# Kernel tuning notes

Measured on AMD Instinct MI355X. Metric: run time of the kernel, lower is better.

The kernel has to match this reference:

```python
import jax, jax.numpy as jnp
import numpy as np
from jax import lax

DIL_R = 2            # dilation_radius
K = 2 * DIL_R + 1    # 5x5 morphology kernel
FOCAL_ALPHA = 0.25
FOCAL_GAMMA = 2.0
BOUNDARY_W = 1.0
IGNORE_IDX = 250


def setup_inputs() -> dict:
    key = jax.random.key(0)
    k1, k2 = jax.random.split(key)
    pred = jax.random.normal(k1, (32, 2, 512, 512), dtype=jnp.float32)
    target = jax.random.randint(k2, (32, 512, 512), 0, 2, dtype=jnp.int64)
    return {"pred": pred, "target": target}


def _boundary_mask(target):
    # labels float, 5x5 all-ones conv with 'same' padding (zero pad),
    # dilated = (conv > 0), eroded = (-conv(-x) > K*K-1) == (conv(x) > K*K-1)
    x = target.astype(jnp.float32)[:, None]                    # [B,1,H,W]
    kern = jnp.ones((1, 1, K, K), dtype=jnp.float32)
    s = lax.conv_general_dilated(x, kern, (1, 1), 'SAME',
                                 dimension_numbers=('NCHW', 'OIHW', 'NCHW'))
    dilated = (s > 0).astype(jnp.float32)
    eroded = (s > (K * K - 1)).astype(jnp.float32)
    return (dilated - eroded)[:, 0]                            # [B,H,W]


def _loss(pred, target, boundary):
    logp = jax.nn.log_softmax(pred, axis=1)                    # [B,2,H,W]
    # per-pixel CE
    ce_pix = -jnp.take_along_axis(logp, target[:, None].astype(jnp.int32), axis=1)[:, 0]  # [B,H,W]
    # main CE with ignore_index=250
    valid = (target != IGNORE_IDX)
    ce_loss = jnp.sum(ce_pix * valid) / jnp.maximum(jnp.sum(valid), 1)
    # focal loss (no ignore, mean over all pixels)
    pt = jnp.exp(-ce_pix)
    focal = jnp.mean(FOCAL_ALPHA * (1.0 - pt) ** FOCAL_GAMMA * ce_pix)
    # boundary dice on class-1 prob
    prob1 = jnp.exp(logp[:, 1])                                # softmax(pred,1)[:,1]
    tgt_f = target.astype(jnp.float32)
    bp = prob1 * boundary
    bt = tgt_f * boundary
    inter = jnp.sum(bp * bt, axis=(1, 2))
    union = jnp.sum(bp, axis=(1, 2)) + jnp.sum(bt, axis=(1, 2))
    dice = 2.0 * inter / (union + 1e-8)
    bdice = 1.0 - jnp.mean(dice)
    return ce_loss + BOUNDARY_W * focal + BOUNDARY_W * bdice


def reference(pred, target):
    boundary = _boundary_mask(target)
    return _loss(pred, target, boundary)
```

## Files before the change

### kernel.cpp

```cpp
#include <hip/hip_runtime.h>
#include <math.h>

#define BATCH 32
#define HH 512
#define WW 512
#define TW 64
#define TH 16
#define HALO 2
#define SW (TW + 2*HALO)
#define SH (TH + 2*HALO)
#define NTILEX (WW / TW)
#define NTILEY (HH / TH)
#define NPIX ((float)BATCH * HH * WW)

#define SLOT(j,b) ((((j) * BATCH) + (b)) * 32)
#define WS_FLOATS (6 * BATCH * 32)

__global__ void zero_ws_kernel(float* ws) {
    int i = blockIdx.x * 256 + threadIdx.x;
    if (i < WS_FLOATS) ws[i] = 0.0f;
}

__global__ __launch_bounds__(256) void bel_main_kernel(
        const float* __restrict__ pred,
        const int*   __restrict__ target,
        float*       __restrict__ ws) {
    __shared__ int   stgt[SH][SW];
    __shared__ int   hsum[SH][TW];
    __shared__ float red[6][4];

    const int tid = threadIdx.x;
    const int bid = blockIdx.x;
    const int bx = bid % NTILEX;
    const int by = (bid / NTILEX) % NTILEY;
    const int b  = bid / (NTILEX * NTILEY);

    const int gx0 = bx * TW - HALO;
    const int gy0 = by * TH - HALO;
    const int tb  = b * HH * WW;

    for (int i = tid; i < SH * SW; i += 256) {
        int r = i / SW, c = i - r * SW;
        int gy = gy0 + r, gx = gx0 + c;
        int v = 0;
        if ((unsigned)gy < (unsigned)HH && (unsigned)gx < (unsigned)WW)
            v = target[tb + gy * WW + gx];
        stgt[r][c] = v;
    }
    __syncthreads();

    for (int i = tid; i < SH * TW; i += 256) {
        int r = i >> 6, c = i & 63;
        hsum[r][c] = stgt[r][c] + stgt[r][c+1] + stgt[r][c+2]
                   + stgt[r][c+3] + stgt[r][c+4];
    }
    __syncthreads();

    const int tx = tid & 63;
    const int ty = tid >> 6;

    float ce_acc = 0.f, cnt_acc = 0.f, focal_acc = 0.f;
    float inter_acc = 0.f, bp_acc = 0.f, bt_acc = 0.f;

    #pragma unroll
    for (int k = 0; k < TH / 4; ++k) {
        const int yl = ty + 4 * k;
        const int y  = by * TH + yl;
        const int x  = bx * TW + tx;

        const int s = hsum[yl][tx] + hsum[yl+1][tx] + hsum[yl+2][tx]
                    + hsum[yl+3][tx] + hsum[yl+4][tx];
        const float bm = (s > 0 && s <= 24) ? 1.0f : 0.0f;

        const int t = stgt[yl + HALO][tx + HALO];

        const int pix = y * WW + x;
        const float p0 = pred[2*tb + pix];
        const float p1 = pred[2*tb + HH*WW + pix];

        const float m   = fmaxf(p0, p1);
        const float d   = fabsf(p0 - p1);
        const float lse = m + __logf(1.0f + __expf(-d));

        const int   tc = (t < 0) ? 0 : ((t > 1) ? 1 : t);
        const float pt_logit = tc ? p1 : p0;
        const float ce = lse - pt_logit;

        const float valid = (t != 250) ? 1.0f : 0.0f;
        ce_acc  += ce * valid;
        cnt_acc += valid;

        const float pt  = __expf(-ce);
        const float omp = 1.0f - pt;
        focal_acc += 0.25f * omp * omp * ce;

        const float prob1 = __expf(p1 - lse);
        const float bp = prob1 * bm;
        const float bt = (float)t * bm;
        inter_acc += bp * bt;
        bp_acc    += bp;
        bt_acc    += bt;
    }

    float vals[6] = {ce_acc, cnt_acc, focal_acc, inter_acc, bp_acc, bt_acc};
    #pragma unroll
    for (int j = 0; j < 6; ++j) {
        float v = vals[j];
        #pragma unroll
        for (int off = 32; off > 0; off >>= 1)
            v += __shfl_down(v, off, 64);
        vals[j] = v;
    }
    const int wave = tid >> 6;
    const int lane = tid & 63;
    if (lane == 0) {
        #pragma unroll
        for (int j = 0; j < 6; ++j) red[j][wave] = vals[j];
    }
    __syncthreads();
    if (tid == 0) {
        #pragma unroll
        for (int j = 0; j < 6; ++j) {
            vals[j] = red[j][0] + red[j][1] + red[j][2] + red[j][3];
            atomicAdd(&ws[SLOT(j, b)], vals[j]);
        }
    }
}

__global__ void bel_finalize_kernel(const float* __restrict__ ws,
                                    float* __restrict__ out) {
    const int t = threadIdx.x;
    float ce_p = 0.f, cnt_p = 0.f, focal_p = 0.f, dice_p = 0.f;
    if (t < BATCH) {
        ce_p    = ws[SLOT(0, t)];
        cnt_p   = ws[SLOT(1, t)];
        focal_p = ws[SLOT(2, t)];
        const float inter = ws[SLOT(3, t)];
        const float uni   = ws[SLOT(4, t)] + ws[SLOT(5, t)];
        dice_p = 2.0f * inter / (uni + 1e-8f);
    }
    #pragma unroll
    for (int off = 32; off > 0; off >>= 1) {
        ce_p    += __shfl_down(ce_p, off, 64);
        cnt_p   += __shfl_down(cnt_p, off, 64);
        focal_p += __shfl_down(focal_p, off, 64);
        dice_p  += __shfl_down(dice_p, off, 64);
    }
    if (t == 0) {
        const float ce_loss = ce_p / fmaxf(cnt_p, 1.0f);
        const float focal   = focal_p / NPIX;
        const float bdice   = 1.0f - dice_p / (float)BATCH;
        out[0] = ce_loss + focal + bdice;
    }
}

extern "C" void kernel_launch(void* const* d_in, const int* in_sizes, int n_in,
                              void* d_out, int out_size, void* d_ws, size_t ws_size,
                              hipStream_t stream) {
    const float* pred   = (const float*)d_in[0];
    const int*   target = (const int*)d_in[1];
    float* ws  = (float*)d_ws;
    float* out = (float*)d_out;

    zero_ws_kernel<<<(WS_FLOATS + 255) / 256, 256, 0, stream>>>(ws);
    bel_main_kernel<<<NTILEX * NTILEY * BATCH, 256, 0, stream>>>(pred, target, ws);
    bel_finalize_kernel<<<1, 64, 0, stream>>>(ws, out);
}
```

Baseline: 134.5 us.

## Use full-row tiles with byte-packed labels and SWAR box sums

Measured after the change: 118.7 us. 1.13x faster.

```diff
diff --git a/kernel.cpp b/kernel.cpp
--- a/kernel.cpp
+++ b/kernel.cpp
@@ -4,14 +4,13 @@
 #define BATCH 32
 #define HH 512
 #define WW 512
-#define TW 64
 #define TH 16
 #define HALO 2
-#define SW (TW + 2*HALO)
-#define SH (TH + 2*HALO)
-#define NTILEX (WW / TW)
-#define NTILEY (HH / TH)
+#define SRH (TH + 2*HALO)
+#define NDW (WW / 4)
+#define CSTRIDE 132
 #define NPIX ((float)BATCH * HH * WW)
+#define HW (HH * WW)
 
 #define SLOT(j,b) ((((j) * BATCH) + (b)) * 32)
 #define WS_FLOATS (6 * BATCH * 32)
@@ -25,104 +24,133 @@
         const float* __restrict__ pred,
         const int*   __restrict__ target,
         float*       __restrict__ ws) {
-    __shared__ int   stgt[SH][SW];
-    __shared__ int   hsum[SH][TW];
+    __shared__ unsigned int t8[SRH][NDW];
+    __shared__ unsigned int csum[TH][CSTRIDE];
     __shared__ float red[6][4];
 
     const int tid = threadIdx.x;
     const int bid = blockIdx.x;
-    const int bx = bid % NTILEX;
-    const int by = (bid / NTILEX) % NTILEY;
-    const int b  = bid / (NTILEX * NTILEY);
+    const int b   = bid >> 5;
+    const int ty  = bid & 31;
+    const int y0  = ty * TH;
+    const size_t tb = (size_t)b * HW;
 
-    const int gx0 = bx * TW - HALO;
-    const int gy0 = by * TH - HALO;
-    const int tb  = b * HH * WW;
+    if (tid < 2 * TH) {
+        int rr = tid >> 1;
+        csum[rr][(tid & 1) ? (NDW + 1) : 0] = 0u;
+    }
 
-    for (int i = tid; i < SH * SW; i += 256) {
-        int r = i / SW, c = i - r * SW;
-        int gy = gy0 + r, gx = gx0 + c;
-        int v = 0;
-        if ((unsigned)gy < (unsigned)HH && (unsigned)gx < (unsigned)WW)
-            v = target[tb + gy * WW + gx];
-        stgt[r][c] = v;
+    #pragma unroll
+    for (int it = 0; it < (SRH * NDW) / 256; ++it) {
+        const int i  = tid + 256 * it;
+        const int r  = i >> 7;
+        const int c4 = i & 127;
+        const int gy = y0 - HALO + r;
+        unsigned int packed = 0u;
+        if ((unsigned)gy < (unsigned)HH) {
+            const int4 v = *(const int4*)(target + tb + ((size_t)gy << 9) + (c4 << 2));
+            packed = (unsigned)v.x | ((unsigned)v.y << 8)
+                   | ((unsigned)v.z << 16) | ((unsigned)v.w << 24);
+        }
+        t8[r][c4] = packed;
     }
     __syncthreads();
 
-    for (int i = tid; i < SH * TW; i += 256) {
-        int r = i >> 6, c = i & 63;
-        hsum[r][c] = stgt[r][c] + stgt[r][c+1] + stgt[r][c+2]
-                   + stgt[r][c+3] + stgt[r][c+4];
+    #pragma unroll
+    for (int it = 0; it < (TH * NDW) / 256; ++it) {
+        const int j = tid + 256 * it;
+        const int r = j >> 7;
+        const int c = j & 127;
+        csum[r][c + 1] = t8[r][c] + t8[r+1][c] + t8[r+2][c]
+                       + t8[r+3][c] + t8[r+4][c];
     }
     __syncthreads();
 
-    const int tx = tid & 63;
-    const int ty = tid >> 6;
+    const float4* __restrict__ pr0 = (const float4*)(pred + tb * 2);
+    const float4* __restrict__ pr1 = (const float4*)(pred + tb * 2 + HW);
 
     float ce_acc = 0.f, cnt_acc = 0.f, focal_acc = 0.f;
     float inter_acc = 0.f, bp_acc = 0.f, bt_acc = 0.f;
 
-    #pragma unroll
-    for (int k = 0; k < TH / 4; ++k) {
-        const int yl = ty + 4 * k;
-        const int y  = by * TH + yl;
-        const int x  = bx * TW + tx;
+    const unsigned long long M5 = 0xFFFFFFFFFFull;
+    const unsigned long long ALL5 = 0x0505050505ull;
 
-        const int s = hsum[yl][tx] + hsum[yl+1][tx] + hsum[yl+2][tx]
-                    + hsum[yl+3][tx] + hsum[yl+4][tx];
-        const float bm = (s > 0 && s <= 24) ? 1.0f : 0.0f;
+    for (int it = 0; it < (TH * NDW) / 256; ++it) {
+        const int j = tid + 256 * it;
+        const int r = j >> 7;
+        const int g = j & 127;
+        const int y = y0 + r;
+        const int fidx = (y << 7) + g;
 
-        const int t = stgt[yl + HALO][tx + HALO];
+        const float4 f0 = pr0[fidx];
+        const float4 f1 = pr1[fidx];
 
-        const int pix = y * WW + x;
-        const float p0 = pred[2*tb + pix];
-        const float p1 = pred[2*tb + HH*WW + pix];
+        const unsigned int L = csum[r][g];
+        const unsigned int M = csum[r][g + 1];
+        const unsigned int R = csum[r][g + 2];
+        const unsigned int tdw = t8[r + HALO][g];
 
-        const float m   = fmaxf(p0, p1);
-        const float d   = fabsf(p0 - p1);
-        const float lse = m + __logf(1.0f + __expf(-d));
+        const unsigned long long lo  = (unsigned long long)L | ((unsigned long long)M << 32);
+        const unsigned long long mid = (unsigned long long)M | ((unsigned long long)R << 32);
 
-        const int   tc = (t < 0) ? 0 : ((t > 1) ? 1 : t);
-        const float pt_logit = tc ? p1 : p0;
-        const float ce = lse - pt_logit;
+        #pragma unroll
+        for (int i = 0; i < 4; ++i) {
+            unsigned long long w;
+            if      (i == 0) w = (lo  >> 16) & M5;
+            else if (i == 1) w = (lo  >> 24) & M5;
+            else if (i == 2) w =  mid        & M5;
+            else             w = (mid >>  8) & M5;
+            const float bm = (w != 0ull && w != ALL5) ? 1.0f : 0.0f;
 
-        const float valid = (t != 250) ? 1.0f : 0.0f;
-        ce_acc  += ce * valid;
-        cnt_acc += valid;
+            const unsigned int tv = (tdw >> (8 * i)) & 0xFFu;
 
-        const float pt  = __expf(-ce);
-        const float omp = 1.0f - pt;
-        focal_acc += 0.25f * omp * omp * ce;
+            const float p0 = (i == 0) ? f0.x : (i == 1) ? f0.y : (i == 2) ? f0.z : f0.w;
+            const float p1 = (i == 0) ? f1.x : (i == 1) ? f1.y : (i == 2) ? f1.z : f1.w;
 
-        const float prob1 = __expf(p1 - lse);
-        const float bp = prob1 * bm;
-        const float bt = (float)t * bm;
-        inter_acc += bp * bt;
-        bp_acc    += bp;
-        bt_acc    += bt;
+            const float d  = p1 - p0;
+            const float e  = __expf(-fabsf(d));
+            const float rz = 1.0f / (1.0f + e);
+            const float pmin = e * rz;
+            const float prob1 = (d >= 0.0f) ? rz : pmin;
+            const float pt = tv ? prob1 : (1.0f - prob1);
+            const float ce = -__logf(pt);
+
+            const float valid = (tv != 250u) ? 1.0f : 0.0f;
+            ce_acc  += ce * valid;
+            cnt_acc += valid;
+
+            const float omp = 1.0f - pt;
+            focal_acc += omp * omp * ce;
+
+            const float bp = prob1 * bm;
+            const float bt = (float)tv * bm;
+            inter_acc += bp * bt;
+            bp_acc    += bp;
+            bt_acc    += bt;
+        }
     }
 
-    float vals[6] = {ce_acc, cnt_acc, focal_acc, inter_acc, bp_acc, bt_acc};
+    float vals[6] = {ce_acc, cnt_acc, focal_acc * 0.25f, inter_acc, bp_acc, bt_acc};
     #pragma unroll
-    for (int j = 0; j < 6; ++j) {
-        float v = vals[j];
+    for (int jj = 0; jj < 6; ++jj) {
+        float v = vals[jj];
         #pragma unroll
         for (int off = 32; off > 0; off >>= 1)
             v += __shfl_down(v, off, 64);
-        vals[j] = v;
+        vals[jj] = v;
     }
     const int wave = tid >> 6;
     const int lane = tid & 63;
     if (lane == 0) {
         #pragma unroll
-        for (int j = 0; j < 6; ++j) red[j][wave] = vals[j];
+        for (int jj = 0; jj < 6; ++jj) red[jj][wave] = vals[jj];
     }
     __syncthreads();
     if (tid == 0) {
         #pragma unroll
-        for (int j = 0; j < 6; ++j) {
-            vals[j] = red[j][0] + red[j][1] + red[j][2] + red[j][3];
-            atomicAdd(&ws[SLOT(j, b)], vals[j]);
+        for (int jj = 0; jj < 6; ++jj) {
+            const float v = red[jj][0] + red[jj][1] + red[jj][2] + red[jj][3];
+            atomicAdd(&ws[SLOT(jj, b)], v);
         }
     }
 }
@@ -163,6 +191,6 @@
     float* out = (float*)d_out;
 
     zero_ws_kernel<<<(WS_FLOATS + 255) / 256, 256, 0, stream>>>(ws);
-    bel_main_kernel<<<NTILEX * NTILEY * BATCH, 256, 0, stream>>>(pred, target, ws);
+    bel_main_kernel<<<BATCH * (HH / TH), 256, 0, stream>>>(pred, target, ws);
     bel_finalize_kernel<<<1, 64, 0, stream>>>(ws, out);
 }
```
